# Kernel tuning notes

Measured on AMD Instinct MI355X. Metric: run time of the kernel, lower is better.

Reference implementation:

```python
import jax, jax.numpy as jnp
import numpy as np

N_NODES = 50000
E_EDGES = 1600000
C_IN = 64
C_OUT = 64
K_CHEB = 3


def _norm(edge_index, edge_weight, n):
    # PyG ChebConv.__norm__ with normalization='sym', lambda_max=2.0:
    # remove self loops, sym-normalized Laplacian scaled by 2/lambda_max, then
    # subtract identity -> L_hat has zero diagonal and off-diag -d^-1/2 w d^-1/2.
    row, col = edge_index[0], edge_index[1]
    mask = row != col
    ew = jnp.where(mask, edge_weight, 0.0)
    deg = jax.ops.segment_sum(ew, row, num_segments=n)  # [N]
    dinv = jnp.where(deg > 0, jax.lax.rsqrt(jnp.where(deg > 0, deg, 1.0)), 0.0)
    wn = -ew * dinv[row] * dinv[col]  # [E], zero on (removed) self loops
    return row, col, wn


def _propagate(x, row, col, wn, n):
    # y = L_hat @ x via edge gather + weighted scatter-add
    return jax.ops.segment_sum(wn[:, None] * x[col], row, num_segments=n)


def _cheb(x, W, b, row, col, wn, n):
    # Chebyshev recursion: Tx0=x, Tx1=L_hat x, Txk = 2 L_hat Tx(k-1) - Tx(k-2)
    out = x @ W[0]
    Tx0, Tx1 = x, None
    if W.shape[0] > 1:
        Tx1 = _propagate(x, row, col, wn, n)
        out = out + Tx1 @ W[1]
    for k in range(2, W.shape[0]):
        Tx2 = 2.0 * _propagate(Tx1, row, col, wn, n) - Tx0
        out = out + Tx2 @ W[k]
        Tx0, Tx1 = Tx1, Tx2
    return out + b


def setup_inputs() -> dict:
    key = jax.random.key(0)
    ks = jax.random.split(key, 40)
    d = {
        'X': jax.random.normal(ks[0], (N_NODES, C_IN), jnp.float32),
        'edge_index': jax.random.randint(ks[1], (2, E_EDGES), 0, N_NODES),
        'edge_weight': jax.random.uniform(ks[2], (E_EDGES,), jnp.float32),
        'H': jax.random.normal(ks[3], (N_NODES, C_OUT), jnp.float32) * 0.1,
        'C': jax.random.normal(ks[4], (N_NODES, C_OUT), jnp.float32) * 0.1,
    }
    i = 5
    sx = 1.0 / np.sqrt(C_IN)
    sh = 1.0 / np.sqrt(C_OUT)
    for nm in ['xi', 'xf', 'xc', 'xo']:
        d['W_' + nm] = jax.random.normal(ks[i], (K_CHEB, C_IN, C_OUT), jnp.float32) * sx; i += 1
        d['bc_' + nm] = jax.random.normal(ks[i], (C_OUT,), jnp.float32) * 0.02; i += 1
    for nm in ['hi', 'hf', 'hc', 'ho']:
        d['W_' + nm] = jax.random.normal(ks[i], (K_CHEB, C_OUT, C_OUT), jnp.float32) * sh; i += 1
        d['bc_' + nm] = jax.random.normal(ks[i], (C_OUT,), jnp.float32) * 0.02; i += 1
    for nm in ['w_ci', 'w_cf', 'w_co', 'b_i', 'b_f', 'b_c', 'b_o']:
        d[nm] = jax.random.normal(ks[i], (1, C_OUT), jnp.float32) * 0.1; i += 1
    return d


def reference(X, edge_index, edge_weight, H, C,
              W_xi, bc_xi, W_xf, bc_xf, W_xc, bc_xc, W_xo, bc_xo,
              W_hi, bc_hi, W_hf, bc_hf, W_hc, bc_hc, W_ho, bc_ho,
              w_ci, w_cf, w_co, b_i, b_f, b_c, b_o):
    n = X.shape[0]
    row, col, wn = _norm(edge_index, edge_weight, n)
    I = jax.nn.sigmoid(_cheb(X, W_xi, bc_xi, row, col, wn, n)
                       + _cheb(H, W_hi, bc_hi, row, col, wn, n)
                       + w_ci * C + b_i)
    Fg = jax.nn.sigmoid(_cheb(X, W_xf, bc_xf, row, col, wn, n)
                        + _cheb(H, W_hf, bc_hf, row, col, wn, n)
                        + w_cf * C + b_f)
    T = jnp.tanh(_cheb(X, W_xc, bc_xc, row, col, wn, n)
                 + _cheb(H, W_hc, bc_hc, row, col, wn, n)
                 + b_c)
    C_new = Fg * C + I * T
    O = jax.nn.sigmoid(_cheb(X, W_xo, bc_xo, row, col, wn, n)
                       + _cheb(H, W_ho, bc_ho, row, col, wn, n)
                       + w_co * C_new + b_o)
    H_new = O * jnp.tanh(C_new)
    return (H_new, C_new)
```

## Files before the change

### kernel.cpp

```cpp
#include <hip/hip_runtime.h>
#include <hip/hip_bf16.h>
#include <math.h>

#define N_NODES 50000
#define E_EDGES 1600000
#define NBKT 196
#define PBLK 400
#define CHUNK 4000

typedef __attribute__((ext_vector_type(8))) short s8v;
typedef __attribute__((ext_vector_type(4))) float f32x4;

#define O_BLKH  0
#define O_BBASE 78592
#define O_BSUM  78848
#define O_CNT   79104
#define O_DINV  129152
#define O_RPTR  179200
#define O_SREC  229248
#define O_SREC2 3429248
#define O_EDGE  O_SREC
#define O_XHB   O_SREC2
#define O_T1B   6629248
#define O_T2B   9829248
#define O_BP    13029248

__device__ __forceinline__ uint pk_bf16(float x, float y) {
  __hip_bfloat16 bx = __float2bfloat16(x), by = __float2bfloat16(y);
  ushort ux = *reinterpret_cast<ushort*>(&bx);
  ushort uy = *reinterpret_cast<ushort*>(&by);
  return ((uint)uy << 16) | (uint)ux;
}

__global__ __launch_bounds__(256) void k_hist(const int* __restrict__ ei,
                                              uint* __restrict__ blkh) {
  __shared__ uint h[NBKT];
  int blk = blockIdx.x, tid = threadIdx.x;
  for (int i = tid; i < NBKT; i += 256) h[i] = 0;
  __syncthreads();
  int e0 = blk * CHUNK;
  for (int i = tid; i < CHUNK; i += 256) {
    int e = e0 + i;
    int r = ei[e], c = ei[E_EDGES + e];
    if (r != c) atomicAdd(&h[r >> 8], 1u);
  }
  __syncthreads();
  for (int i = tid; i < NBKT; i += 256) blkh[i * PBLK + blk] = h[i];
}

__global__ __launch_bounds__(256) void k_bsum_scan(uint* __restrict__ blkh,
                                                   uint* __restrict__ bsum) {
  __shared__ uint sh[512];
  int b = blockIdx.x, t = threadIdx.x;
  uint v0 = (t < PBLK) ? blkh[b * PBLK + t] : 0u;
  uint v1 = (t + 256 < PBLK) ? blkh[b * PBLK + t + 256] : 0u;
  sh[t] = v0; sh[t + 256] = v1;
  __syncthreads();
  for (int off = 1; off < 512; off <<= 1) {
    uint x0 = sh[t], x1 = sh[t + 256];
    uint a0 = (t >= off) ? sh[t - off] : 0u;
    uint a1 = (t + 256 >= off) ? sh[t + 256 - off] : 0u;
    __syncthreads();
    sh[t] = x0 + a0; sh[t + 256] = x1 + a1;
    __syncthreads();
  }
  if (t < PBLK) blkh[b * PBLK + t] = sh[t] - v0;
  if (t + 256 < PBLK) blkh[b * PBLK + t + 256] = sh[t + 256] - v1;
  if (t == 0) bsum[b] = sh[511];
}

__global__ __launch_bounds__(256) void k_bscan(const uint* __restrict__ bsum,
                                               uint* __restrict__ bbase) {
  __shared__ uint sh[256];
  int t = threadIdx.x;
  uint v = (t < NBKT) ? bsum[t] : 0u;
  sh[t] = v;
  __syncthreads();
  for (int off = 1; off < 256; off <<= 1) {
    uint a = (t >= off) ? sh[t - off] : 0u;
    __syncthreads();
    sh[t] += a;
    __syncthreads();
  }
  if (t < NBKT) bbase[t] = sh[t] - v;
  if (t == 255) bbase[NBKT] = sh[255];
}

__global__ __launch_bounds__(256) void k_scatter_b(const int* __restrict__ ei,
                                                   const float* __restrict__ ew,
                                                   const uint* __restrict__ off,
                                                   const uint* __restrict__ bbase,
                                                   unsigned long long* __restrict__ srec) {
  __shared__ uint cur[NBKT];
  int blk = blockIdx.x, tid = threadIdx.x;
  for (int i = tid; i < NBKT; i += 256) cur[i] = off[i * PBLK + blk] + bbase[i];
  __syncthreads();
  int e0 = blk * CHUNK;
  for (int i = tid; i < CHUNK; i += 256) {
    int e = e0 + i;
    int r = ei[e], c = ei[E_EDGES + e];
    if (r != c) {
      uint pos = atomicAdd(&cur[r >> 8], 1u);
      srec[pos] = ((unsigned long long)(r & 255) << 48) |
                  ((unsigned long long)(uint)c << 32) |
                  (unsigned long long)__float_as_uint(ew[e]);
    }
  }
}

__global__ __launch_bounds__(256) void k_csr(const unsigned long long* __restrict__ srec,
                                             const uint* __restrict__ bbase,
                                             unsigned long long* __restrict__ srec2,
                                             int* __restrict__ cnt, float* __restrict__ dinv,
                                             int* __restrict__ rptr) {
  __shared__ uint hc[256], hs[256], cur[256], wsum[4];
  int b = blockIdx.x, t = threadIdx.x;
  uint start = bbase[b], endv = bbase[b + 1];
  hc[t] = 0; hs[t] = 0;
  __syncthreads();
  for (uint i = start + t; i < endv; i += 256) {
    unsigned long long rec = srec[i];
    int rl = (int)(rec >> 48);
    float w = __uint_as_float((uint)rec);
    atomicAdd(&hc[rl], 1u);
    atomicAdd(&hs[rl], (uint)(w * 1048576.0f + 0.5f));
  }
  __syncthreads();
  int lane = t & 63, wid = t >> 6;
  uint myc = hc[t];
  uint x = myc;
#pragma unroll
  for (int off = 1; off < 64; off <<= 1) {
    uint y = __shfl_up(x, off);
    if (lane >= off) x += y;
  }
  if (lane == 63) wsum[wid] = x;
  __syncthreads();
  uint woff = 0;
#pragma unroll
  for (int j = 0; j < 4; ++j) if (j < wid) woff += wsum[j];
  uint excl = woff + x - myc;
  int row = b * 256 + t;
  if (row < N_NODES) {
    float d = (float)hs[t] * (1.0f / 1048576.0f);
    dinv[row] = d > 0.f ? rsqrtf(d) : 0.f;
    cnt[row] = (int)myc;
    rptr[row] = (int)(start + excl);
  }
  cur[t] = start + excl;
  __syncthreads();
  for (uint i = start + t; i < endv; i += 256) {
    unsigned long long rec = srec[i];
    int rl = (int)(rec >> 48);
    uint pos = atomicAdd(&cur[rl], 1u);
    srec2[pos] = rec;
  }
}

__global__ __launch_bounds__(256) void k_finalize(const unsigned long long* __restrict__ srec2,
                                                  const uint* __restrict__ bbase,
                                                  const float* __restrict__ dinv,
                                                  uint* __restrict__ edges) {
  int b = blockIdx.x, t = threadIdx.x;
  uint start = bbase[b], endv = bbase[b + 1];
  for (uint i = start + t; i < endv; i += 256) {
    unsigned long long rec = srec2[i];
    int rl = (int)(rec >> 48);
    int c = (int)((rec >> 32) & 0xffff);
    float w = __uint_as_float((uint)rec);
    int r = b * 256 + rl;
    float wn = -w * dinv[r] * dinv[c];
    __hip_bfloat16 bw = __float2bfloat16(wn);
    edges[i] = ((uint)c << 16) | (uint)*reinterpret_cast<ushort*>(&bw);
  }
}

__global__ void k_xhb(const float* __restrict__ X, const float* __restrict__ Hm,
                      uint* __restrict__ XHb) {
  int t = blockIdx.x * blockDim.x + threadIdx.x;
  if (t >= N_NODES * 64) return;
  int n = t >> 6, q = t & 63;
  float2 v = (q < 32) ? *(const float2*)(X + (long)n * 64 + q * 2)
                      : *(const float2*)(Hm + (long)n * 64 + (q - 32) * 2);
  XHb[t] = pk_bf16(v.x, v.y);
}

__global__ __launch_bounds__(256) void k_spmm2b(
    const uint* __restrict__ src, const uint* __restrict__ other,
    float alpha, float beta,
    const int* __restrict__ rptr, const int* __restrict__ cnt,
    const uint* __restrict__ edges, uint* __restrict__ out) {
  int wid = threadIdx.x >> 6, lane = threadIdx.x & 63;
  int row = blockIdx.x * 4 + wid;
  if (row >= N_NODES) return;
  int start = rptr[row], n = cnt[row];
  float ax = 0.f, ay = 0.f;
  for (int base = 0; base < n; base += 64) {
    int rem = n - base;
    int m = rem < 64 ? rem : 64;
    uint rec = (lane < m) ? edges[start + base + lane] : 0u;
    int j = 0;
    for (; j + 4 <= m; j += 4) {
#pragma unroll
      for (int u = 0; u < 4; ++u) {
        uint r = __shfl(rec, j + u);
        int cc = (int)(r >> 16);
        float ww = __uint_as_float(r << 16);
        uint z = src[cc * 64 + lane];
        ax = fmaf(ww, __uint_as_float(z << 16), ax);
        ay = fmaf(ww, __uint_as_float(z & 0xffff0000u), ay);
      }
    }
    for (; j < m; ++j) {
      uint r = __shfl(rec, j);
      int cc = (int)(r >> 16);
      float ww = __uint_as_float(r << 16);
      uint z = src[cc * 64 + lane];
      ax = fmaf(ww, __uint_as_float(z << 16), ax);
      ay = fmaf(ww, __uint_as_float(z & 0xffff0000u), ay);
    }
  }
  float ox = alpha * ax, oy = alpha * ay;
  if (beta != 0.f) {
    uint ov = other[row * 64 + lane];
    ox += beta * __uint_as_float(ov << 16);
    oy += beta * __uint_as_float(ov & 0xffff0000u);
  }
  out[row * 64 + lane] = pk_bf16(ox, oy);
}

__global__ void k_pack(const float* __restrict__ Wxi, const float* __restrict__ Wxf,
                       const float* __restrict__ Wxc, const float* __restrict__ Wxo,
                       const float* __restrict__ Whi, const float* __restrict__ Whf,
                       const float* __restrict__ Whc, const float* __restrict__ Who,
                       ushort* __restrict__ Bp) {
  int idx = blockIdx.x * blockDim.x + threadIdx.x;
  if (idx >= 12 * 16 * 64 * 8) return;
  int j = idx & 7;
  int lane = (idx >> 3) & 63;
  int c = (idx >> 9) & 15;
  int t = idx >> 13;
  int k = t * 32 + (lane >> 4) * 8 + j;
  int col = c * 16 + (lane & 15);
  int g = col >> 6, oc = col & 63;
  int s = k >> 6, kk = k & 63, ord = s >> 1;
  const float* Wx[4] = {Wxi, Wxf, Wxc, Wxo};
  const float* Wh[4] = {Whi, Whf, Whc, Who};
  const float* W = (s & 1) ? Wh[g] : Wx[g];
  float v = W[(ord * 64 + kk) * 64 + oc];
  __hip_bfloat16 b = __float2bfloat16(v);
  Bp[idx] = *reinterpret_cast<ushort*>(&b);
}

__device__ __forceinline__ float frcp(float x) { return __builtin_amdgcn_rcpf(x); }

__global__ __launch_bounds__(256) void k_mfma_lstm(
    const ushort* __restrict__ XHb, const ushort* __restrict__ T1b,
    const ushort* __restrict__ T2b, const float* __restrict__ C,
    const ushort* __restrict__ Bp,
    const float* __restrict__ bxi, const float* __restrict__ bxf,
    const float* __restrict__ bxc, const float* __restrict__ bxo,
    const float* __restrict__ bhi, const float* __restrict__ bhf,
    const float* __restrict__ bhc, const float* __restrict__ bho,
    const float* __restrict__ wci, const float* __restrict__ wcf, const float* __restrict__ wco,
    const float* __restrict__ bi, const float* __restrict__ bf_,
    const float* __restrict__ bc_, const float* __restrict__ bo,
    float* __restrict__ Hout, float* __restrict__ Cout) {
  __shared__ ushort bsh[2][8192];
  int lane = threadIdx.x & 63, wid = threadIdx.x >> 6;
  int row0 = blockIdx.x * 64 + wid * 16;
  int ar = row0 + (lane & 15);
  if (ar > N_NODES - 1) ar = N_NODES - 1;
  long abase = (long)ar * 128 + (lane >> 4) * 8;

#define STAGE(buf, t)                                                          \
  {                                                                            \
    _Pragma("unroll") for (int q = 0; q < 4; ++q) {                            \
      int seg = wid * 4 + q;                                                   \
      __builtin_amdgcn_global_load_lds(                                        \
          (const __attribute__((address_space(1))) uint*)(Bp + (t)*8192 +     \
                                                          seg * 512 + lane * 8),\
          (__attribute__((address_space(3))) uint*)&bsh[buf][seg * 512],       \
          16, 0, 0);                                                           \
    }                                                                          \
  }

  STAGE(0, 0)

  s8v a[12];
#pragma unroll
  for (int q = 0; q < 4; ++q) a[q] = *(const s8v*)(XHb + abase + q * 32);
#pragma unroll
  for (int q = 0; q < 4; ++q) a[4 + q] = *(const s8v*)(T1b + abase + q * 32);
#pragma unroll
  for (int q = 0; q < 4; ++q) a[8 + q] = *(const s8v*)(T2b + abase + q * 32);

  f32x4 acc[16];
#pragma unroll
  for (int c = 0; c < 16; ++c) acc[c] = {0.f, 0.f, 0.f, 0.f};

#pragma unroll
  for (int t = 0; t < 12; ++t) {
    int buf = t & 1;
    __syncthreads();
    if (t < 11) STAGE(buf ^ 1, t + 1)
    const ushort* bp = &bsh[buf][lane * 8];
#pragma unroll
    for (int c = 0; c < 16; ++c) {
      s8v b = *(const s8v*)(bp + c * 512);
      acc[c] = __builtin_amdgcn_mfma_f32_16x16x32_bf16(a[t], b, acc[c], 0, 0, 0);
    }
  }
#undef STAGE

  int rbase = row0 + ((lane >> 4) << 2);
  int ocl = lane & 15;
#pragma unroll
  for (int j = 0; j < 4; ++j) {
    int oc = j * 16 + ocl;
    float bI = bxi[oc] + bhi[oc] + bi[oc];
    float bF = bxf[oc] + bhf[oc] + bf_[oc];
    float bT = bxc[oc] + bhc[oc] + bc_[oc];
    float bO = bxo[oc] + bho[oc] + bo[oc];
    float wcI = wci[oc], wcF = wcf[oc], wcO = wco[oc];
#pragma unroll
    for (int r = 0; r < 4; ++r) {
      int row = rbase + r;
      if (row < N_NODES) {
        float cv = C[(long)row * 64 + oc];
        float I = frcp(1.f + __expf(-(acc[j][r] + bI + wcI * cv)));
        float F = frcp(1.f + __expf(-(acc[4 + j][r] + bF + wcF * cv)));
        float e2 = __expf(2.f * (acc[8 + j][r] + bT));
        float T = 1.f - 2.f * frcp(e2 + 1.f);
        float cn = F * cv + I * T;
        float O = frcp(1.f + __expf(-(acc[12 + j][r] + bO + wcO * cn)));
        float e2c = __expf(2.f * cn);
        float tc = 1.f - 2.f * frcp(e2c + 1.f);
        Hout[(long)row * 64 + oc] = O * tc;
        Cout[(long)row * 64 + oc] = cn;
      }
    }
  }
}

extern "C" void kernel_launch(void* const* d_in, const int* in_sizes, int n_in,
                              void* d_out, int out_size, void* d_ws, size_t ws_size,
                              hipStream_t stream) {
  (void)in_sizes; (void)n_in; (void)out_size; (void)ws_size;
  const float* X   = (const float*)d_in[0];
  const int*   ei  = (const int*)d_in[1];
  const float* ew  = (const float*)d_in[2];
  const float* H   = (const float*)d_in[3];
  const float* C   = (const float*)d_in[4];
  const float* Wxi = (const float*)d_in[5];
  const float* bxi = (const float*)d_in[6];
  const float* Wxf = (const float*)d_in[7];
  const float* bxf = (const float*)d_in[8];
  const float* Wxc = (const float*)d_in[9];
  const float* bxc = (const float*)d_in[10];
  const float* Wxo = (const float*)d_in[11];
  const float* bxo = (const float*)d_in[12];
  const float* Whi = (const float*)d_in[13];
  const float* bhi = (const float*)d_in[14];
  const float* Whf = (const float*)d_in[15];
  const float* bhf = (const float*)d_in[16];
  const float* Whc = (const float*)d_in[17];
  const float* bhc = (const float*)d_in[18];
  const float* Who = (const float*)d_in[19];
  const float* bho = (const float*)d_in[20];
  const float* wci = (const float*)d_in[21];
  const float* wcf = (const float*)d_in[22];
  const float* wco = (const float*)d_in[23];
  const float* bi  = (const float*)d_in[24];
  const float* bf_ = (const float*)d_in[25];
  const float* bc_ = (const float*)d_in[26];
  const float* bo  = (const float*)d_in[27];

  float* ws = (float*)d_ws;
  uint*   blkh  = (uint*)(ws + O_BLKH);
  uint*   bbase = (uint*)(ws + O_BBASE);
  uint*   bsum  = (uint*)(ws + O_BSUM);
  int*    cnt   = (int*)(ws + O_CNT);
  float*  dinv  = ws + O_DINV;
  int*    rptr  = (int*)(ws + O_RPTR);
  unsigned long long* srec  = (unsigned long long*)(ws + O_SREC);
  unsigned long long* srec2 = (unsigned long long*)(ws + O_SREC2);
  uint*   edges = (uint*)(ws + O_EDGE);
  uint*   XHb   = (uint*)(ws + O_XHB);
  uint*   T1b   = (uint*)(ws + O_T1B);
  uint*   T2b   = (uint*)(ws + O_T2B);
  ushort* Bp    = (ushort*)(ws + O_BP);

  float* Hout = (float*)d_out;
  float* Cout = Hout + N_NODES * 64;

  k_hist<<<PBLK, 256, 0, stream>>>(ei, blkh);
  k_bsum_scan<<<NBKT, 256, 0, stream>>>(blkh, bsum);
  k_bscan<<<1, 256, 0, stream>>>(bsum, bbase);
  k_scatter_b<<<PBLK, 256, 0, stream>>>(ei, ew, blkh, bbase, srec);
  k_csr<<<NBKT, 256, 0, stream>>>(srec, bbase, srec2, cnt, dinv, rptr);
  k_finalize<<<NBKT, 256, 0, stream>>>(srec2, bbase, dinv, edges);
  k_xhb<<<(N_NODES * 64 + 255) / 256, 256, 0, stream>>>(X, H, XHb);
  k_pack<<<(12 * 16 * 64 * 8 + 255) / 256, 256, 0, stream>>>(Wxi, Wxf, Wxc, Wxo,
                                                             Whi, Whf, Whc, Who, Bp);
  int spmm_grid = (N_NODES + 3) / 4;
  k_spmm2b<<<spmm_grid, 256, 0, stream>>>(XHb, XHb, 1.f, 0.f, rptr, cnt, edges, T1b);
  k_spmm2b<<<spmm_grid, 256, 0, stream>>>(T1b, XHb, 2.f, -1.f, rptr, cnt, edges, T2b);
  k_mfma_lstm<<<(N_NODES + 63) / 64, 256, 0, stream>>>(
      (const ushort*)XHb, (const ushort*)T1b, (const ushort*)T2b, C, Bp,
      bxi, bxf, bxc, bxo, bhi, bhf, bhc, bho,
      wci, wcf, wco, bi, bf_, bc_, bo, Hout, Cout);
}
```

Baseline: 223.9 us.

## Split feature buffers into four channel quarters and parallelize SpMM per quarter

Stores the bf16 X/H, T1 and T2 buffers as four column-quarter planes of 16 uints per node rather than one 64-uint row. The SpMM now assigns each (row-group, quarter) pair to its own block, with four edge streams per wave reduced by shuffles, so each gather touches a 64-byte slice and a quarter plane is more likely to stay in cache. The MFMA kernel reads A fragments from the planar layout and loads all B fragments from LDS before issuing the next stage. The cost is four times as many SpMM blocks, each re-reading the edge lists, plus a cross-lane reduction.

```diff
diff --git a/kernel.cpp b/kernel.cpp
--- a/kernel.cpp
+++ b/kernel.cpp
@@ -20,9 +20,9 @@
 #define O_SREC  229248
 #define O_SREC2 3429248
 #define O_EDGE  O_SREC
-#define O_XHB   O_SREC2
-#define O_T1B   6629248
-#define O_T2B   9829248
+#define O_XHQ   O_SREC2
+#define O_T1Q   6629248
+#define O_T2Q   9829248
 #define O_BP    13029248
 
 __device__ __forceinline__ uint pk_bf16(float x, float y) {
@@ -176,57 +176,49 @@
 }
 
 __global__ void k_xhb(const float* __restrict__ X, const float* __restrict__ Hm,
-                      uint* __restrict__ XHb) {
+                      uint* __restrict__ XHq) {
   int t = blockIdx.x * blockDim.x + threadIdx.x;
   if (t >= N_NODES * 64) return;
-  int n = t >> 6, q = t & 63;
-  float2 v = (q < 32) ? *(const float2*)(X + (long)n * 64 + q * 2)
-                      : *(const float2*)(Hm + (long)n * 64 + (q - 32) * 2);
-  XHb[t] = pk_bf16(v.x, v.y);
-}
-
-__global__ __launch_bounds__(256) void k_spmm2b(
+  int n = t >> 6, j = t & 63;
+  float2 v = (j < 32) ? *(const float2*)(X + (long)n * 64 + j * 2)
+                      : *(const float2*)(Hm + (long)n * 64 + (j - 32) * 2);
+  XHq[((long)(j >> 4) * N_NODES + n) * 16 + (j & 15)] = pk_bf16(v.x, v.y);
+}
+
+__global__ __launch_bounds__(256) void k_spmm2q(
     const uint* __restrict__ src, const uint* __restrict__ other,
     float alpha, float beta,
     const int* __restrict__ rptr, const int* __restrict__ cnt,
     const uint* __restrict__ edges, uint* __restrict__ out) {
+  int bid = blockIdx.x;
+  int q = (bid & 7) >> 1;
+  int rg = ((bid >> 3) << 1) + (bid & 1);
   int wid = threadIdx.x >> 6, lane = threadIdx.x & 63;
-  int row = blockIdx.x * 4 + wid;
-  if (row >= N_NODES) return;
+  int row = rg * 4 + wid;
+  int ch = lane & 15, es = lane >> 4;
+  const uint* sq = src + (long)q * (N_NODES * 16);
   int start = rptr[row], n = cnt[row];
   float ax = 0.f, ay = 0.f;
-  for (int base = 0; base < n; base += 64) {
-    int rem = n - base;
-    int m = rem < 64 ? rem : 64;
-    uint rec = (lane < m) ? edges[start + base + lane] : 0u;
-    int j = 0;
-    for (; j + 4 <= m; j += 4) {
-#pragma unroll
-      for (int u = 0; u < 4; ++u) {
-        uint r = __shfl(rec, j + u);
-        int cc = (int)(r >> 16);
-        float ww = __uint_as_float(r << 16);
-        uint z = src[cc * 64 + lane];
-        ax = fmaf(ww, __uint_as_float(z << 16), ax);
-        ay = fmaf(ww, __uint_as_float(z & 0xffff0000u), ay);
-      }
+  for (int j = es; j < n; j += 4) {
+    uint rec = edges[start + j];
+    int cc = (int)(rec >> 16);
+    float ww = __uint_as_float(rec << 16);
+    uint z = sq[cc * 16 + ch];
+    ax = fmaf(ww, __uint_as_float(z << 16), ax);
+    ay = fmaf(ww, __uint_as_float(z & 0xffff0000u), ay);
+  }
+  ax += __shfl_xor(ax, 16); ay += __shfl_xor(ay, 16);
+  ax += __shfl_xor(ax, 32); ay += __shfl_xor(ay, 32);
+  if (es == 0) {
+    long o = (long)q * (N_NODES * 16) + (long)row * 16 + ch;
+    float ox = alpha * ax, oy = alpha * ay;
+    if (beta != 0.f) {
+      uint ov = other[o];
+      ox += beta * __uint_as_float(ov << 16);
+      oy += beta * __uint_as_float(ov & 0xffff0000u);
     }
-    for (; j < m; ++j) {
-      uint r = __shfl(rec, j);
-      int cc = (int)(r >> 16);
-      float ww = __uint_as_float(r << 16);
-      uint z = src[cc * 64 + lane];
-      ax = fmaf(ww, __uint_as_float(z << 16), ax);
-      ay = fmaf(ww, __uint_as_float(z & 0xffff0000u), ay);
-    }
-  }
-  float ox = alpha * ax, oy = alpha * ay;
-  if (beta != 0.f) {
-    uint ov = other[row * 64 + lane];
-    ox += beta * __uint_as_float(ov << 16);
-    oy += beta * __uint_as_float(ov & 0xffff0000u);
-  }
-  out[row * 64 + lane] = pk_bf16(ox, oy);
+    out[o] = pk_bf16(ox, oy);
+  }
 }
 
 __global__ void k_pack(const float* __restrict__ Wxi, const float* __restrict__ Wxf,
@@ -255,8 +247,8 @@
 __device__ __forceinline__ float frcp(float x) { return __builtin_amdgcn_rcpf(x); }
 
 __global__ __launch_bounds__(256) void k_mfma_lstm(
-    const ushort* __restrict__ XHb, const ushort* __restrict__ T1b,
-    const ushort* __restrict__ T2b, const float* __restrict__ C,
+    const uint* __restrict__ XHq, const uint* __restrict__ T1q,
+    const uint* __restrict__ T2q, const float* __restrict__ C,
     const ushort* __restrict__ Bp,
     const float* __restrict__ bxi, const float* __restrict__ bxf,
     const float* __restrict__ bxc, const float* __restrict__ bxo,
@@ -271,12 +263,11 @@
   int row0 = blockIdx.x * 64 + wid * 16;
   int ar = row0 + (lane & 15);
   if (ar > N_NODES - 1) ar = N_NODES - 1;
-  long abase = (long)ar * 128 + (lane >> 4) * 8;
 
 #define STAGE(buf, t)                                                          \
   {                                                                            \
-    _Pragma("unroll") for (int q = 0; q < 4; ++q) {                            \
-      int seg = wid * 4 + q;                                                   \
+    _Pragma("unroll") for (int qq = 0; qq < 4; ++qq) {                         \
+      int seg = wid * 4 + qq;                                                  \
       __builtin_amdgcn_global_load_lds(                                        \
           (const __attribute__((address_space(1))) uint*)(Bp + (t)*8192 +     \
                                                           seg * 512 + lane * 8),\
@@ -287,13 +278,17 @@
 
   STAGE(0, 0)
 
+  const ushort* XHs = (const ushort*)XHq;
+  const ushort* T1s = (const ushort*)T1q;
+  const ushort* T2s = (const ushort*)T2q;
   s8v a[12];
 #pragma unroll
-  for (int q = 0; q < 4; ++q) a[q] = *(const s8v*)(XHb + abase + q * 32);
-#pragma unroll
-  for (int q = 0; q < 4; ++q) a[4 + q] = *(const s8v*)(T1b + abase + q * 32);
-#pragma unroll
-  for (int q = 0; q < 4; ++q) a[8 + q] = *(const s8v*)(T2b + abase + q * 32);
+  for (int q = 0; q < 4; ++q) {
+    long off = ((long)q * N_NODES + ar) * 32 + (lane >> 4) * 8;
+    a[q]     = *(const s8v*)(XHs + off);
+    a[4 + q] = *(const s8v*)(T1s + off);
+    a[8 + q] = *(const s8v*)(T2s + off);
+  }
 
   f32x4 acc[16];
 #pragma unroll
@@ -303,13 +298,14 @@
   for (int t = 0; t < 12; ++t) {
     int buf = t & 1;
     __syncthreads();
+    s8v bfr[16];
+#pragma unroll
+    for (int c = 0; c < 16; ++c)
+      bfr[c] = *(const s8v*)(&bsh[buf][c * 512 + lane * 8]);
     if (t < 11) STAGE(buf ^ 1, t + 1)
-    const ushort* bp = &bsh[buf][lane * 8];
-#pragma unroll
-    for (int c = 0; c < 16; ++c) {
-      s8v b = *(const s8v*)(bp + c * 512);
-      acc[c] = __builtin_amdgcn_mfma_f32_16x16x32_bf16(a[t], b, acc[c], 0, 0, 0);
-    }
+#pragma unroll
+    for (int c = 0; c < 16; ++c)
+      acc[c] = __builtin_amdgcn_mfma_f32_16x16x32_bf16(a[t], bfr[c], acc[c], 0, 0, 0);
   }
 #undef STAGE
 
@@ -386,9 +382,9 @@
   unsigned long long* srec  = (unsigned long long*)(ws + O_SREC);
   unsigned long long* srec2 = (unsigned long long*)(ws + O_SREC2);
   uint*   edges = (uint*)(ws + O_EDGE);
-  uint*   XHb   = (uint*)(ws + O_XHB);
-  uint*   T1b   = (uint*)(ws + O_T1B);
-  uint*   T2b   = (uint*)(ws + O_T2B);
+  uint*   XHq   = (uint*)(ws + O_XHQ);
+  uint*   T1q   = (uint*)(ws + O_T1Q);
+  uint*   T2q   = (uint*)(ws + O_T2Q);
   ushort* Bp    = (ushort*)(ws + O_BP);
 
   float* Hout = (float*)d_out;
@@ -400,14 +396,13 @@
   k_scatter_b<<<PBLK, 256, 0, stream>>>(ei, ew, blkh, bbase, srec);
   k_csr<<<NBKT, 256, 0, stream>>>(srec, bbase, srec2, cnt, dinv, rptr);
   k_finalize<<<NBKT, 256, 0, stream>>>(srec2, bbase, dinv, edges);
-  k_xhb<<<(N_NODES * 64 + 255) / 256, 256, 0, stream>>>(X, H, XHb);
+  k_xhb<<<(N_NODES * 64 + 255) / 256, 256, 0, stream>>>(X, H, XHq);
   k_pack<<<(12 * 16 * 64 * 8 + 255) / 256, 256, 0, stream>>>(Wxi, Wxf, Wxc, Wxo,
                                                              Whi, Whf, Whc, Who, Bp);
-  int spmm_grid = (N_NODES + 3) / 4;
-  k_spmm2b<<<spmm_grid, 256, 0, stream>>>(XHb, XHb, 1.f, 0.f, rptr, cnt, edges, T1b);
-  k_spmm2b<<<spmm_grid, 256, 0, stream>>>(T1b, XHb, 2.f, -1.f, rptr, cnt, edges, T2b);
+  k_spmm2q<<<N_NODES, 256, 0, stream>>>(XHq, XHq, 1.f, 0.f, rptr, cnt, edges, T1q);
+  k_spmm2q<<<N_NODES, 256, 0, stream>>>(T1q, XHq, 2.f, -1.f, rptr, cnt, edges, T2q);
   k_mfma_lstm<<<(N_NODES + 63) / 64, 256, 0, stream>>>(
-      (const ushort*)XHb, (const ushort*)T1b, (const ushort*)T2b, C, Bp,
+      XHq, T1q, T2q, C, Bp,
       bxi, bxf, bxc, bxo, bhi, bhf, bhc, bho,
       wci, wcf, wco, bi, bf_, bc_, bo, Hout, Cout);
 }
```

Measured after the change: 386.4 us. +72.6%, slower.

## Split SpMM wave across two edges with 8-byte gathers; shrink MFMA LSTM blocks

Applied to the files above, without the earlier changes.

The SpMM kernel now has each half-wave handle alternate edges, with every lane loading two packed bf16 words (uint2) per gather. Partial sums are combined with a cross-half shuffle and only the lower half writes. This halves the number of serial gather iterations per row and widens each memory access, at the cost of extra registers and a reduction step. The MFMA LSTM kernel moves to 128-thread blocks of 32 rows and preloads all B fragments from LDS before issuing the next stage's async copy, trading more redundant B staging for more blocks and better overlap.

```diff
diff --git a/kernel.cpp b/kernel.cpp
--- a/kernel.cpp
+++ b/kernel.cpp
@@ -194,39 +194,54 @@
   int row = blockIdx.x * 4 + wid;
   if (row >= N_NODES) return;
   int start = rptr[row], n = cnt[row];
-  float ax = 0.f, ay = 0.f;
+  int half = lane >> 5;
+  int l5 = lane & 31;
+  float ax = 0.f, ay = 0.f, bx = 0.f, by = 0.f;
   for (int base = 0; base < n; base += 64) {
-    int rem = n - base;
-    int m = rem < 64 ? rem : 64;
+    int m = n - base; if (m > 64) m = 64;
     uint rec = (lane < m) ? edges[start + base + lane] : 0u;
+    int iters = (m + 1) >> 1;
     int j = 0;
-    for (; j + 4 <= m; j += 4) {
+    for (; j + 4 <= iters; j += 4) {
 #pragma unroll
       for (int u = 0; u < 4; ++u) {
-        uint r = __shfl(rec, j + u);
+        uint r = __shfl(rec, 2 * (j + u) + half);
         int cc = (int)(r >> 16);
         float ww = __uint_as_float(r << 16);
-        uint z = src[cc * 64 + lane];
-        ax = fmaf(ww, __uint_as_float(z << 16), ax);
-        ay = fmaf(ww, __uint_as_float(z & 0xffff0000u), ay);
+        uint2 z = *(const uint2*)(src + cc * 64 + (l5 << 1));
+        ax = fmaf(ww, __uint_as_float(z.x << 16), ax);
+        ay = fmaf(ww, __uint_as_float(z.x & 0xffff0000u), ay);
+        bx = fmaf(ww, __uint_as_float(z.y << 16), bx);
+        by = fmaf(ww, __uint_as_float(z.y & 0xffff0000u), by);
       }
     }
-    for (; j < m; ++j) {
-      uint r = __shfl(rec, j);
+    for (; j < iters; ++j) {
+      uint r = __shfl(rec, 2 * j + half);
       int cc = (int)(r >> 16);
       float ww = __uint_as_float(r << 16);
-      uint z = src[cc * 64 + lane];
-      ax = fmaf(ww, __uint_as_float(z << 16), ax);
-      ay = fmaf(ww, __uint_as_float(z & 0xffff0000u), ay);
+      uint2 z = *(const uint2*)(src + cc * 64 + (l5 << 1));
+      ax = fmaf(ww, __uint_as_float(z.x << 16), ax);
+      ay = fmaf(ww, __uint_as_float(z.x & 0xffff0000u), ay);
+      bx = fmaf(ww, __uint_as_float(z.y << 16), bx);
+      by = fmaf(ww, __uint_as_float(z.y & 0xffff0000u), by);
     }
   }
-  float ox = alpha * ax, oy = alpha * ay;
-  if (beta != 0.f) {
-    uint ov = other[row * 64 + lane];
-    ox += beta * __uint_as_float(ov << 16);
-    oy += beta * __uint_as_float(ov & 0xffff0000u);
-  }
-  out[row * 64 + lane] = pk_bf16(ox, oy);
+  ax += __shfl_xor(ax, 32); ay += __shfl_xor(ay, 32);
+  bx += __shfl_xor(bx, 32); by += __shfl_xor(by, 32);
+  if (half == 0) {
+    long o = (long)row * 64 + (l5 << 1);
+    float ox = alpha * ax, oy = alpha * ay;
+    float px = alpha * bx, py = alpha * by;
+    if (beta != 0.f) {
+      uint2 ov = *(const uint2*)(other + o);
+      ox += beta * __uint_as_float(ov.x << 16);
+      oy += beta * __uint_as_float(ov.x & 0xffff0000u);
+      px += beta * __uint_as_float(ov.y << 16);
+      py += beta * __uint_as_float(ov.y & 0xffff0000u);
+    }
+    uint2 w2; w2.x = pk_bf16(ox, oy); w2.y = pk_bf16(px, py);
+    *(uint2*)(out + o) = w2;
+  }
 }
 
 __global__ void k_pack(const float* __restrict__ Wxi, const float* __restrict__ Wxf,
@@ -254,9 +269,9 @@
 
 __device__ __forceinline__ float frcp(float x) { return __builtin_amdgcn_rcpf(x); }
 
-__global__ __launch_bounds__(256) void k_mfma_lstm(
-    const ushort* __restrict__ XHb, const ushort* __restrict__ T1b,
-    const ushort* __restrict__ T2b, const float* __restrict__ C,
+__global__ __launch_bounds__(128) void k_mfma_lstm(
+    const uint* __restrict__ XHb, const uint* __restrict__ T1b,
+    const uint* __restrict__ T2b, const float* __restrict__ C,
     const ushort* __restrict__ Bp,
     const float* __restrict__ bxi, const float* __restrict__ bxf,
     const float* __restrict__ bxc, const float* __restrict__ bxo,
@@ -268,15 +283,14 @@
     float* __restrict__ Hout, float* __restrict__ Cout) {
   __shared__ ushort bsh[2][8192];
   int lane = threadIdx.x & 63, wid = threadIdx.x >> 6;
-  int row0 = blockIdx.x * 64 + wid * 16;
+  int row0 = blockIdx.x * 32 + wid * 16;
   int ar = row0 + (lane & 15);
   if (ar > N_NODES - 1) ar = N_NODES - 1;
-  long abase = (long)ar * 128 + (lane >> 4) * 8;
 
 #define STAGE(buf, t)                                                          \
   {                                                                            \
-    _Pragma("unroll") for (int q = 0; q < 4; ++q) {                            \
-      int seg = wid * 4 + q;                                                   \
+    _Pragma("unroll") for (int qq = 0; qq < 8; ++qq) {                         \
+      int seg = wid * 8 + qq;                                                  \
       __builtin_amdgcn_global_load_lds(                                        \
           (const __attribute__((address_space(1))) uint*)(Bp + (t)*8192 +     \
                                                           seg * 512 + lane * 8),\
@@ -287,13 +301,17 @@
 
   STAGE(0, 0)
 
+  const ushort* XHs = (const ushort*)XHb;
+  const ushort* T1s = (const ushort*)T1b;
+  const ushort* T2s = (const ushort*)T2b;
+  long abase = (long)ar * 128 + (lane >> 4) * 8;
   s8v a[12];
 #pragma unroll
-  for (int q = 0; q < 4; ++q) a[q] = *(const s8v*)(XHb + abase + q * 32);
-#pragma unroll
-  for (int q = 0; q < 4; ++q) a[4 + q] = *(const s8v*)(T1b + abase + q * 32);
-#pragma unroll
-  for (int q = 0; q < 4; ++q) a[8 + q] = *(const s8v*)(T2b + abase + q * 32);
+  for (int q = 0; q < 4; ++q) a[q] = *(const s8v*)(XHs + abase + q * 32);
+#pragma unroll
+  for (int q = 0; q < 4; ++q) a[4 + q] = *(const s8v*)(T1s + abase + q * 32);
+#pragma unroll
+  for (int q = 0; q < 4; ++q) a[8 + q] = *(const s8v*)(T2s + abase + q * 32);
 
   f32x4 acc[16];
 #pragma unroll
@@ -303,13 +321,14 @@
   for (int t = 0; t < 12; ++t) {
     int buf = t & 1;
     __syncthreads();
+    s8v bfr[16];
+#pragma unroll
+    for (int c = 0; c < 16; ++c)
+      bfr[c] = *(const s8v*)(&bsh[buf][c * 512 + lane * 8]);
     if (t < 11) STAGE(buf ^ 1, t + 1)
-    const ushort* bp = &bsh[buf][lane * 8];
-#pragma unroll
-    for (int c = 0; c < 16; ++c) {
-      s8v b = *(const s8v*)(bp + c * 512);
-      acc[c] = __builtin_amdgcn_mfma_f32_16x16x32_bf16(a[t], b, acc[c], 0, 0, 0);
-    }
+#pragma unroll
+    for (int c = 0; c < 16; ++c)
+      acc[c] = __builtin_amdgcn_mfma_f32_16x16x32_bf16(a[t], bfr[c], acc[c], 0, 0, 0);
   }
 #undef STAGE
 
@@ -406,8 +425,8 @@
   int spmm_grid = (N_NODES + 3) / 4;
   k_spmm2b<<<spmm_grid, 256, 0, stream>>>(XHb, XHb, 1.f, 0.f, rptr, cnt, edges, T1b);
   k_spmm2b<<<spmm_grid, 256, 0, stream>>>(T1b, XHb, 2.f, -1.f, rptr, cnt, edges, T2b);
-  k_mfma_lstm<<<(N_NODES + 63) / 64, 256, 0, stream>>>(
-      (const ushort*)XHb, (const ushort*)T1b, (const ushort*)T2b, C, Bp,
+  k_mfma_lstm<<<(N_NODES + 31) / 32, 128, 0, stream>>>(
+      XHb, T1b, T2b, C, Bp,
       bxi, bxf, bxc, bxo, bhi, bhf, bhc, bho,
       wci, wcf, wco, bi, bf_, bc_, bo, Hout, Cout);
 }
```

Result: faster. 218.3 us (-2.5%).
